# Kernel tuning notes

Hardware: AMD Instinct MI355X
Metric: run time of the kernel (lower is better)

## Reference

```python
import jax, jax.numpy as jnp
import numpy as np

B, C, N, T = 16, 32, 1024, 128
R = 10  # low-rank bottleneck of W1/W2


def setup_inputs() -> dict:
    key = jax.random.key(0)
    k1, k2, k3, k4 = jax.random.split(key, 4)
    x = jax.random.normal(k1, (B, C, N, T), dtype=jnp.float32)
    W1 = jax.random.normal(k2, (R, N), dtype=jnp.float32) * 0.05
    W2 = jax.random.normal(k3, (R, N), dtype=jnp.float32) * 0.05
    alpha = jax.random.normal(k4, (C,), dtype=jnp.float32) * 0.1
    return {"x": x, "W1": W1, "W2": W2, "alpha": alpha}


def reference(x, W1, W2, alpha):
    # k = q = einsum('bint,i->btn', x, alpha): contract channels -> [B, T, N]
    k = jnp.einsum('bcnt,c->btn', x, alpha)
    # low-rank bilinear scores: (k @ W1^T) @ (k @ W2^T)^T -> [B, T, T]
    kw1 = jnp.einsum('btn,rn->btr', k, W1)   # [B, T, R]
    qw2 = jnp.einsum('btn,rn->btr', k, W2)   # [B, T, R]
    scores = jnp.einsum('btr,bsr->bts', kw1, qw2)  # [B, T, T]
    att = jax.nn.softmax(scores, axis=-1)
    # weighted sum over time: einsum('bti,bcni->bcnt', att, x)
    return jnp.einsum('bts,bcns->bcnt', att, x)
```

## Files before the change

kernel.cpp:

```cpp
#include <hip/hip_runtime.h>
#include <hip/hip_bf16.h>


#define B_ 16
#define C_ 32
#define N_ 1024
#define T_ 128
#define R_ 10

typedef __bf16 bf16x8 __attribute__((ext_vector_type(8)));
typedef __bf16 bf16x4 __attribute__((ext_vector_type(4)));
typedef float f32x4 __attribute__((ext_vector_type(4)));

__device__ __forceinline__ void lds_barrier() {
    asm volatile("s_waitcnt lgkmcnt(0)" ::: "memory");
    __builtin_amdgcn_s_barrier();
    asm volatile("" ::: "memory");
}

__global__ __launch_bounds__(256) void k_reduce_c(const float* __restrict__ x,
                                                  const float* __restrict__ alpha,
                                                  float* __restrict__ k) {
    int bid = blockIdx.x;
    int b   = bid >> 7;
    int nc  = bid & 127;
    int tid = threadIdx.x;
    int nl  = tid >> 5;
    int lc  = tid & 31;
    int n   = nc * 8 + nl;
    const float4* xb = reinterpret_cast<const float4*>(
        x + ((size_t)(b * C_) * N_ + n) * T_) + lc;
    float4 acc = {0.f, 0.f, 0.f, 0.f};
    #pragma unroll 8
    for (int c = 0; c < C_; ++c) {
        float a = alpha[c];
        float4 v = xb[(size_t)c * (N_ * T_ / 4)];
        acc.x += a * v.x; acc.y += a * v.y; acc.z += a * v.z; acc.w += a * v.w;
    }
    reinterpret_cast<float4*>(k + ((size_t)b * N_ + n) * T_)[lc] = acc;
}

__global__ __launch_bounds__(128) void kw_partial2(const float* __restrict__ k,
                                                   const float* __restrict__ W1,
                                                   const float* __restrict__ W2,
                                                   float* __restrict__ p1,
                                                   float* __restrict__ p2) {
    __shared__ float wl[32][20];
    int bid = blockIdx.x;
    int b   = bid >> 5;
    int ch  = bid & 31;
    int n0  = ch * 32;
    int t   = threadIdx.x;
    for (int i = t; i < 32 * 20; i += 128) {
        int nl = i & 31, q = i >> 5;
        wl[nl][q] = (q < 10) ? W1[q * N_ + n0 + nl] : W2[(q - 10) * N_ + n0 + nl];
    }
    __syncthreads();
    float a1[R_] = {}, a2[R_] = {};
    const float* kb = k + ((size_t)b * N_ + n0) * T_ + t;
    #pragma unroll 2
    for (int g = 0; g < 4; ++g) {
        float kv[8];
        #pragma unroll
        for (int j = 0; j < 8; ++j) kv[j] = kb[(g * 8 + j) * T_];
        #pragma unroll
        for (int j = 0; j < 8; ++j) {
            int nl = g * 8 + j;
            #pragma unroll
            for (int r = 0; r < R_; ++r) {
                a1[r] += kv[j] * wl[nl][r];
                a2[r] += kv[j] * wl[nl][10 + r];
            }
        }
    }
    #pragma unroll
    for (int r = 0; r < R_; ++r) {
        size_t o = (((size_t)b * R_ + r) * 32 + ch) * T_ + t;
        p1[o] = a1[r];
        p2[o] = a2[r];
    }
}

__global__ __launch_bounds__(128) void kw_reduce(const float* __restrict__ p1,
                                                 const float* __restrict__ p2,
                                                 float* __restrict__ kwc) {
    int bid = blockIdx.x;
    int b = bid / 20;
    int q = bid - b * 20;
    int w = q / 10;
    int r = q - w * 10;
    int t = threadIdx.x;
    const float* src = (w ? p2 : p1) + (((size_t)b * R_ + r) * 32) * T_ + t;
    float s = 0.f;
    #pragma unroll
    for (int ch = 0; ch < 32; ++ch) s += src[ch * T_];
    kwc[(((size_t)b * 2 + w) * R_ + r) * T_ + t] = s;
}

__global__ __launch_bounds__(128) void scores_softmax(const float* __restrict__ kwc,
                                                      __bf16* __restrict__ att) {
    __shared__ __align__(16) float kw1s[T_][12];
    __shared__ __align__(16) float kw2s[T_][12];
    __shared__ float sc[T_][T_ + 1];
    int b = blockIdx.x;
    int t = threadIdx.x;
    const float* kb = kwc + (size_t)b * 2 * R_ * T_;
    #pragma unroll
    for (int r = 0; r < R_; ++r) {
        kw1s[t][r] = kb[r * T_ + t];
        kw2s[t][r] = kb[(R_ + r) * T_ + t];
    }
    __syncthreads();
    float myw[R_];
    #pragma unroll
    for (int r = 0; r < R_; ++r) myw[r] = kw1s[t][r];
    float mx = -1e30f;
    for (int s = 0; s < T_; ++s) {
        float wv[12];
        const float4* qr = reinterpret_cast<const float4*>(&kw2s[s][0]);
        #pragma unroll
        for (int q = 0; q < 3; ++q) *reinterpret_cast<float4*>(&wv[q * 4]) = qr[q];
        float v = 0.f;
        #pragma unroll
        for (int r = 0; r < R_; ++r) v += myw[r] * wv[r];
        sc[t][s] = v;
        mx = fmaxf(mx, v);
    }
    float sum = 0.f;
    for (int s = 0; s < T_; ++s) {
        float e = __expf(sc[t][s] - mx);
        sc[t][s] = e;
        sum += e;
    }
    float inv = 1.0f / sum;
    __bf16* arow = att + ((size_t)b * T_ + t) * T_;
    for (int s8 = 0; s8 < T_; s8 += 8) {
        bf16x8 hv;
        #pragma unroll
        for (int q = 0; q < 8; ++q) hv[q] = (__bf16)(sc[t][s8 + q] * inv);
        *reinterpret_cast<bf16x8*>(arow + s8) = hv;
    }
}

__global__ __launch_bounds__(256, 2) void out_gemm4(const float* __restrict__ x,
                                                    const __bf16* __restrict__ att,
                                                    float* __restrict__ out) {
    __shared__ __align__(16) __bf16 attl[T_][T_];
    __shared__ __align__(16) __bf16 xsl[2][64][T_];
    int bid = blockIdx.x;
    int sg  = bid & 3;
    int c   = (bid >> 2) & 31;
    int b   = bid >> 7;
    int tid = threadIdx.x;
    char* attb = (char*)&attl[0][0];
    size_t slab0 = ((size_t)(b * C_ + c) * N_ + (sg * 4) * 64) * T_;

    const uint4* ga = reinterpret_cast<const uint4*>(att + (size_t)b * T_ * T_);
    uint4 ar[8];
    #pragma unroll
    for (int i = 0; i < 8; ++i) ar[i] = ga[i * 256 + tid];
    const float4* gx0 = reinterpret_cast<const float4*>(x + slab0);
    float4 xr[8];
    #pragma unroll
    for (int j = 0; j < 8; ++j) xr[j] = gx0[j * 256 + tid];
    #pragma unroll
    for (int i = 0; i < 8; ++i) {
        int e = i * 256 + tid, row = e >> 4;
        int bc = ((e & 15) * 16) ^ ((row & 7) << 4);
        *reinterpret_cast<uint4*>(attb + row * 256 + bc) = ar[i];
    }
    {
        char* xb0 = (char*)&xsl[0][0][0];
        #pragma unroll
        for (int j = 0; j < 8; ++j) {
            int e = j * 256 + tid, row = e >> 5;
            bf16x4 hv = {(__bf16)xr[j].x, (__bf16)xr[j].y, (__bf16)xr[j].z, (__bf16)xr[j].w};
            *reinterpret_cast<bf16x4*>(xb0 + row * 256 + (((e & 31) * 8) ^ ((row & 7) << 4))) = hv;
        }
    }
    lds_barrier();

    int wave = tid >> 6, lane = tid & 63;
    int r16 = lane & 15, g = lane >> 4;
    int wt = wave & 1, wn = wave >> 1;
    int swz = (r16 & 7) << 4;

    #pragma unroll
    for (int i = 0; i < 4; ++i) {
        float4 xn[8];
        if (i < 3) {
            const float4* gxn = reinterpret_cast<const float4*>(
                x + slab0 + ((size_t)(i + 1) * 64) * T_);
            #pragma unroll
            for (int j = 0; j < 8; ++j) xn[j] = gxn[j * 256 + tid];
        }
        const char* xbb = (const char*)&xsl[i & 1][0][0];
        f32x4 acc[2][4] = {};
        #pragma unroll
        for (int ks = 0; ks < 4; ++ks) {
            int kc = ks * 64 + g * 16;
            bf16x8 a[4], bx[2];
            #pragma unroll
            for (int tt = 0; tt < 4; ++tt)
                a[tt] = *reinterpret_cast<const bf16x8*>(
                    attb + (wt * 64 + tt * 16 + r16) * 256 + (kc ^ swz));
            #pragma unroll
            for (int nn = 0; nn < 2; ++nn)
                bx[nn] = *reinterpret_cast<const bf16x8*>(
                    xbb + (wn * 32 + nn * 16 + r16) * 256 + (kc ^ swz));
            #pragma unroll
            for (int nn = 0; nn < 2; ++nn)
                #pragma unroll
                for (int tt = 0; tt < 4; ++tt)
                    acc[nn][tt] = __builtin_amdgcn_mfma_f32_16x16x32_bf16(
                        a[tt], bx[nn], acc[nn][tt], 0, 0, 0);
        }
        float* o = out + slab0 + ((size_t)i * 64) * T_;
        #pragma unroll
        for (int nn = 0; nn < 2; ++nn) {
            int n_l = wn * 32 + nn * 16 + r16;
            #pragma unroll
            for (int tt = 0; tt < 4; ++tt)
                *reinterpret_cast<f32x4*>(
                    o + (size_t)n_l * T_ + (wt * 64 + tt * 16 + g * 4)) = acc[nn][tt];
        }
        if (i < 3) {
            char* xw = (char*)&xsl[(i + 1) & 1][0][0];
            #pragma unroll
            for (int j = 0; j < 8; ++j) {
                int e = j * 256 + tid, row = e >> 5;
                bf16x4 hv = {(__bf16)xn[j].x, (__bf16)xn[j].y,
                             (__bf16)xn[j].z, (__bf16)xn[j].w};
                *reinterpret_cast<bf16x4*>(
                    xw + row * 256 + (((e & 31) * 8) ^ ((row & 7) << 4))) = hv;
            }
            lds_barrier();
        }
    }
}

extern "C" void kernel_launch(void* const* d_in, const int* in_sizes, int n_in,
                              void* d_out, int out_size, void* d_ws, size_t ws_size,
                              hipStream_t stream) {
    const float* x     = (const float*)d_in[0];
    const float* W1    = (const float*)d_in[1];
    const float* W2    = (const float*)d_in[2];
    const float* alpha = (const float*)d_in[3];
    float* out = (float*)d_out;

    float* k    = (float*)d_ws;
    float* p1   = k   + (size_t)B_ * N_ * T_;
    float* p2   = p1  + (size_t)B_ * R_ * 32 * T_;
    float* kwc  = p2  + (size_t)B_ * R_ * 32 * T_;
    __bf16* att = (__bf16*)(kwc + (size_t)B_ * 2 * R_ * T_);

    k_reduce_c   <<<dim3(B_ * (N_ / 8)), dim3(256), 0, stream>>>(x, alpha, k);
    kw_partial2  <<<dim3(B_ * 32),       dim3(128), 0, stream>>>(k, W1, W2, p1, p2);
    kw_reduce    <<<dim3(B_ * 20),       dim3(128), 0, stream>>>(p1, p2, kwc);
    scores_softmax<<<dim3(B_),           dim3(128), 0, stream>>>(kwc, att);
    out_gemm4    <<<dim3(B_ * C_ * 4),   dim3(256), 0, stream>>>(x, att, out);
}
```

Baseline: 186.1 us.

## Emit pre-swizzled bf16 copy of x in reduction pass and feed GEMM from it

The channel-reduction kernel now also writes a bf16, LDS-swizzled copy of x into workspace. The output GEMM then loads that copy straight into shared memory, skipping the fp32 load and conversion, and walks its blocks in reverse order so it may hit recently written data in cache. The separate kw_reduce launch is folded into the softmax kernel. The cost is an extra 128 MB write and a large workspace requirement, with a fallback to the old path when the workspace is too small.

```diff
diff --git a/kernel.cpp b/kernel.cpp
--- a/kernel.cpp
+++ b/kernel.cpp
@@ -16,6 +16,36 @@
     asm volatile("s_waitcnt lgkmcnt(0)" ::: "memory");
     __builtin_amdgcn_s_barrier();
     asm volatile("" ::: "memory");
+}
+
+__global__ __launch_bounds__(256) void k_reduce_cw(const float* __restrict__ x,
+                                                   const float* __restrict__ alpha,
+                                                   float* __restrict__ k,
+                                                   __bf16* __restrict__ xb16) {
+    int bid = blockIdx.x;
+    int b   = bid >> 7;
+    int nc  = bid & 127;
+    int tid = threadIdx.x;
+    int nl  = tid >> 5;
+    int lc  = tid & 31;
+    int n   = nc * 8 + nl;
+    int slab = nc >> 3;
+    int row  = ((nc & 7) << 3) + nl;
+    int wbyte = (lc * 8) ^ (nl << 4);
+    const float4* xb = reinterpret_cast<const float4*>(
+        x + ((size_t)(b * C_) * N_ + n) * T_) + lc;
+    char* xwb = (char*)xb16 +
+        (((size_t)(b * C_) * 16 + slab) * 64 + row) * 256 + wbyte;
+    float4 acc = {0.f, 0.f, 0.f, 0.f};
+    #pragma unroll 8
+    for (int c = 0; c < C_; ++c) {
+        float a = alpha[c];
+        float4 v = xb[(size_t)c * (N_ * T_ / 4)];
+        acc.x += a * v.x; acc.y += a * v.y; acc.z += a * v.z; acc.w += a * v.w;
+        bf16x4 hv = {(__bf16)v.x, (__bf16)v.y, (__bf16)v.z, (__bf16)v.w};
+        *reinterpret_cast<bf16x4*>(xwb + (size_t)c * (16 * 64 * 256)) = hv;
+    }
+    reinterpret_cast<float4*>(k + ((size_t)b * N_ + n) * T_)[lc] = acc;
 }
 
 __global__ __launch_bounds__(256) void k_reduce_c(const float* __restrict__ x,
@@ -81,34 +111,22 @@
     }
 }
 
-__global__ __launch_bounds__(128) void kw_reduce(const float* __restrict__ p1,
-                                                 const float* __restrict__ p2,
-                                                 float* __restrict__ kwc) {
-    int bid = blockIdx.x;
-    int b = bid / 20;
-    int q = bid - b * 20;
-    int w = q / 10;
-    int r = q - w * 10;
-    int t = threadIdx.x;
-    const float* src = (w ? p2 : p1) + (((size_t)b * R_ + r) * 32) * T_ + t;
-    float s = 0.f;
-    #pragma unroll
-    for (int ch = 0; ch < 32; ++ch) s += src[ch * T_];
-    kwc[(((size_t)b * 2 + w) * R_ + r) * T_ + t] = s;
-}
-
-__global__ __launch_bounds__(128) void scores_softmax(const float* __restrict__ kwc,
-                                                      __bf16* __restrict__ att) {
+__global__ __launch_bounds__(128) void scores_softmax3(const float* __restrict__ p1,
+                                                       const float* __restrict__ p2,
+                                                       __bf16* __restrict__ att) {
     __shared__ __align__(16) float kw1s[T_][12];
     __shared__ __align__(16) float kw2s[T_][12];
     __shared__ float sc[T_][T_ + 1];
     int b = blockIdx.x;
     int t = threadIdx.x;
-    const float* kb = kwc + (size_t)b * 2 * R_ * T_;
     #pragma unroll
     for (int r = 0; r < R_; ++r) {
-        kw1s[t][r] = kb[r * T_ + t];
-        kw2s[t][r] = kb[(R_ + r) * T_ + t];
+        float s1 = 0.f, s2 = 0.f;
+        const float* q1 = p1 + (((size_t)b * R_ + r) * 32) * T_ + t;
+        const float* q2 = p2 + (((size_t)b * R_ + r) * 32) * T_ + t;
+        #pragma unroll 4
+        for (int ch = 0; ch < 32; ++ch) { s1 += q1[ch * T_]; s2 += q2[ch * T_]; }
+        kw1s[t][r] = s1; kw2s[t][r] = s2;
     }
     __syncthreads();
     float myw[R_];
@@ -139,6 +157,93 @@
         #pragma unroll
         for (int q = 0; q < 8; ++q) hv[q] = (__bf16)(sc[t][s8 + q] * inv);
         *reinterpret_cast<bf16x8*>(arow + s8) = hv;
+    }
+}
+
+__global__ __launch_bounds__(256, 2) void out_gemm6(const __bf16* __restrict__ xb16,
+                                                    const __bf16* __restrict__ att,
+                                                    float* __restrict__ out) {
+    __shared__ __align__(16) __bf16 attl[T_][T_];
+    __shared__ __align__(16) __bf16 xsl[2][64][T_];
+    int rbid = (int)gridDim.x - 1 - (int)blockIdx.x;
+    int sg  = rbid & 3;
+    int c   = (rbid >> 2) & 31;
+    int b   = rbid >> 7;
+    int tid = threadIdx.x;
+    char* attb = (char*)&attl[0][0];
+
+    const uint4* ga = reinterpret_cast<const uint4*>(att + (size_t)b * T_ * T_);
+    uint4 ar[8];
+    #pragma unroll
+    for (int i = 0; i < 8; ++i) ar[i] = ga[i * 256 + tid];
+    const uint4* gx0 = reinterpret_cast<const uint4*>(xb16) +
+                       ((size_t)((b * C_ + c) * 16 + sg * 4)) * 1024;
+    uint4 xr[4];
+    #pragma unroll
+    for (int q = 0; q < 4; ++q) xr[q] = gx0[q * 256 + tid];
+    #pragma unroll
+    for (int i = 0; i < 8; ++i) {
+        int e = i * 256 + tid, row = e >> 4;
+        int bc = ((e & 15) * 16) ^ ((row & 7) << 4);
+        *reinterpret_cast<uint4*>(attb + row * 256 + bc) = ar[i];
+    }
+    {
+        uint4* lb = reinterpret_cast<uint4*>(&xsl[0][0][0]);
+        #pragma unroll
+        for (int q = 0; q < 4; ++q) lb[q * 256 + tid] = xr[q];
+    }
+    lds_barrier();
+
+    int wave = tid >> 6, lane = tid & 63;
+    int r16 = lane & 15, g = lane >> 4;
+    int wt = wave & 1, wn = wave >> 1;
+    int swz = (r16 & 7) << 4;
+    size_t slab0 = ((size_t)(b * C_ + c) * N_ + sg * 256) * T_;
+
+    #pragma unroll
+    for (int i = 0; i < 4; ++i) {
+        uint4 xn[4];
+        if (i < 3) {
+            const uint4* gxn = gx0 + (size_t)(i + 1) * 1024;
+            #pragma unroll
+            for (int q = 0; q < 4; ++q) xn[q] = gxn[q * 256 + tid];
+        }
+        const char* xbb = (const char*)&xsl[i & 1][0][0];
+        f32x4 acc[2][4] = {};
+        #pragma unroll
+        for (int ks = 0; ks < 4; ++ks) {
+            int kc = ks * 64 + g * 16;
+            bf16x8 a[4], bx[2];
+            #pragma unroll
+            for (int tt = 0; tt < 4; ++tt)
+                a[tt] = *reinterpret_cast<const bf16x8*>(
+                    attb + (wt * 64 + tt * 16 + r16) * 256 + (kc ^ swz));
+            #pragma unroll
+            for (int nn = 0; nn < 2; ++nn)
+                bx[nn] = *reinterpret_cast<const bf16x8*>(
+                    xbb + (wn * 32 + nn * 16 + r16) * 256 + (kc ^ swz));
+            #pragma unroll
+            for (int nn = 0; nn < 2; ++nn)
+                #pragma unroll
+                for (int tt = 0; tt < 4; ++tt)
+                    acc[nn][tt] = __builtin_amdgcn_mfma_f32_16x16x32_bf16(
+                        a[tt], bx[nn], acc[nn][tt], 0, 0, 0);
+        }
+        float* o = out + slab0 + ((size_t)i * 64) * T_;
+        #pragma unroll
+        for (int nn = 0; nn < 2; ++nn) {
+            int n_l = wn * 32 + nn * 16 + r16;
+            #pragma unroll
+            for (int tt = 0; tt < 4; ++tt)
+                *reinterpret_cast<f32x4*>(
+                    o + (size_t)n_l * T_ + (wt * 64 + tt * 16 + g * 4)) = acc[nn][tt];
+        }
+        if (i < 3) {
+            uint4* lw = reinterpret_cast<uint4*>(&xsl[(i + 1) & 1][0][0]);
+            #pragma unroll
+            for (int q = 0; q < 4; ++q) lw[q * 256 + tid] = xn[q];
+            lds_barrier();
+        }
     }
 }
 
@@ -248,15 +353,25 @@
     const float* alpha = (const float*)d_in[3];
     float* out = (float*)d_out;
 
+    const size_t KSZ = (size_t)B_ * N_ * T_;
+    const size_t PSZ = (size_t)B_ * R_ * 32 * T_;
+    const size_t ASZ = (size_t)B_ * T_ * T_;
     float* k    = (float*)d_ws;
-    float* p1   = k   + (size_t)B_ * N_ * T_;
-    float* p2   = p1  + (size_t)B_ * R_ * 32 * T_;
-    float* kwc  = p2  + (size_t)B_ * R_ * 32 * T_;
-    __bf16* att = (__bf16*)(kwc + (size_t)B_ * 2 * R_ * T_);
-
-    k_reduce_c   <<<dim3(B_ * (N_ / 8)), dim3(256), 0, stream>>>(x, alpha, k);
-    kw_partial2  <<<dim3(B_ * 32),       dim3(128), 0, stream>>>(k, W1, W2, p1, p2);
-    kw_reduce    <<<dim3(B_ * 20),       dim3(128), 0, stream>>>(p1, p2, kwc);
-    scores_softmax<<<dim3(B_),           dim3(128), 0, stream>>>(kwc, att);
-    out_gemm4    <<<dim3(B_ * C_ * 4),   dim3(256), 0, stream>>>(x, att, out);
-}
+    float* p1   = k + KSZ;
+    float* p2   = p1 + PSZ;
+    __bf16* att = (__bf16*)(p2 + PSZ);
+    __bf16* xb16 = (__bf16*)((char*)(att + ASZ) + ((16 - (((size_t)(att + ASZ)) & 15)) & 15));
+    size_t need = (char*)(xb16 + (size_t)B_ * C_ * N_ * T_) - (char*)d_ws;
+
+    if (ws_size >= need) {
+        k_reduce_cw    <<<dim3(B_ * (N_ / 8)), dim3(256), 0, stream>>>(x, alpha, k, xb16);
+        kw_partial2    <<<dim3(B_ * 32),       dim3(128), 0, stream>>>(k, W1, W2, p1, p2);
+        scores_softmax3<<<dim3(B_),            dim3(128), 0, stream>>>(p1, p2, att);
+        out_gemm6      <<<dim3(B_ * C_ * 4),   dim3(256), 0, stream>>>(xb16, att, out);
+    } else {
+        k_reduce_c     <<<dim3(B_ * (N_ / 8)), dim3(256), 0, stream>>>(x, alpha, k);
+        kw_partial2    <<<dim3(B_ * 32),       dim3(128), 0, stream>>>(k, W1, W2, p1, p2);
+        scores_softmax3<<<dim3(B_),            dim3(128), 0, stream>>>(p1, p2, att);
+        out_gemm4      <<<dim3(B_ * C_ * 4),   dim3(256), 0, stream>>>(x, att, out);
+    }
+}
```

New measurement: 216.7 us. +16.4%, slower.
